# Optimization experiments

Measured on AMD Instinct MI355X. Metric: run time of the kernel, lower is better.

The kernel has to match this reference:

```python
import jax, jax.numpy as jnp
import numpy as np

B, S, D, H = 8, 1024, 1024, 16
HD = D // H  # head_dim = 64


def setup_inputs() -> dict:
    key = jax.random.key(0)
    ks = jax.random.split(key, 5)
    scale = 1.0 / np.sqrt(D)
    return {
        "x": jax.random.normal(ks[0], (B, S, D), dtype=jnp.float32),
        "wq": jax.random.normal(ks[1], (D, D), dtype=jnp.float32) * scale,
        "wk": jax.random.normal(ks[2], (D, D), dtype=jnp.float32) * scale,
        "wv": jax.random.normal(ks[3], (D, D), dtype=jnp.float32) * scale,
        "wo": jax.random.normal(ks[4], (D, D), dtype=jnp.float32) * scale,
    }


def reference(x, wq, wk, wv, wo):
    b, s, d = x.shape
    # nn.Linear: y = x @ W.T  (weights stored [out, in])
    q = (x @ wq.T).reshape(b, s, H, HD).transpose(0, 2, 1, 3)  # [b,h,s,hd]
    k = (x @ wk.T).reshape(b, s, H, HD).transpose(0, 2, 1, 3)
    v = (x @ wv.T).reshape(b, s, H, HD).transpose(0, 2, 1, 3)
    scores = jnp.einsum("bhqd,bhkd->bhqk", q, k) / jnp.sqrt(jnp.float32(HD))
    attn = jax.nn.softmax(scores, axis=-1)  # dropout p=0.0 -> identity
    out = jnp.einsum("bhqk,bhkd->bhqd", attn, v)
    out = out.transpose(0, 2, 1, 3).reshape(b, s, d)
    return out @ wo.T
```

## Files before the change

kernel.cpp:

```cpp
#include <hip/hip_runtime.h>
#include <hip/hip_bf16.h>
#include <math.h>

#define BB 8
#define SS 1024
#define DD 1024
#define HH 16
#define HDIM 64
#define MM (BB * SS)
#define QSCALE 0.1803368801111204f

typedef __attribute__((ext_vector_type(8))) short s8v;
typedef __attribute__((ext_vector_type(4))) short s4v;
typedef __attribute__((ext_vector_type(4))) float f4v;

#define GLD16(g, l)                                                            \
  __builtin_amdgcn_global_load_lds(                                            \
      (const __attribute__((address_space(1))) void*)(g),                      \
      (__attribute__((address_space(3))) void*)(l), 16, 0, 0)

__device__ __forceinline__ unsigned short bf16_ru(float f) {
  return (unsigned short)((__float_as_uint(f) + 0x8000u) >> 16);
}

__global__ void cast_kernel(const float* __restrict__ in,
                            __hip_bfloat16* __restrict__ out, int n) {
  int i = blockIdx.x * blockDim.x + threadIdx.x;
  int stride = gridDim.x * blockDim.x;
  for (int idx = i * 4; idx < n; idx += stride * 4) {
    float4 f = *(const float4*)&in[idx];
    out[idx + 0] = __float2bfloat16(f.x);
    out[idx + 1] = __float2bfloat16(f.y);
    out[idx + 2] = __float2bfloat16(f.z);
    out[idx + 3] = __float2bfloat16(f.w);
  }
}

template <int MODE>
__global__ __launch_bounds__(256, 2) void gemm_bt(
    const __hip_bfloat16* __restrict__ A, const __hip_bfloat16* __restrict__ Bm,
    float* __restrict__ Cf, __hip_bfloat16* __restrict__ Qo,
    __hip_bfloat16* __restrict__ Ko, __hip_bfloat16* __restrict__ Vt) {
  __shared__ __hip_bfloat16 sA[128 * 32];
  __shared__ __hip_bfloat16 sB[128 * 32];

  const int tid = threadIdx.x;
  const int wave = tid >> 6;
  const int lane = tid & 63;
  const int l15 = lane & 15;
  const int quad = lane >> 4;

  const int m0 = blockIdx.y * 128;
  const int n0 = blockIdx.x * 128;
  const int wm = (wave >> 1) * 64;
  const int wn = (wave & 1) * 64;

  f4v acc[4][4];
#pragma unroll
  for (int i = 0; i < 4; ++i)
#pragma unroll
    for (int j = 0; j < 4; ++j) acc[i][j] = {0.f, 0.f, 0.f, 0.f};

  for (int kt = 0; kt < DD / 32; ++kt) {
    const int k0 = kt * 32;
    __syncthreads();
#pragma unroll
    for (int r = 0; r < 2; ++r) {
      int e = r * 2048 + tid * 8;
      int row = e >> 5, col = e & 31;
      GLD16(A + (size_t)(m0 + row) * DD + k0 + col, &sA[r * 2048 + wave * 512]);
      GLD16(Bm + (size_t)(n0 + row) * DD + k0 + col, &sB[r * 2048 + wave * 512]);
    }
    __syncthreads();

    s8v af[4], bf[4];
#pragma unroll
    for (int i = 0; i < 4; ++i)
      af[i] = *(const s8v*)&sA[(wm + i * 16 + l15) * 32 + quad * 8];
#pragma unroll
    for (int j = 0; j < 4; ++j)
      bf[j] = *(const s8v*)&sB[(wn + j * 16 + l15) * 32 + quad * 8];
#pragma unroll
    for (int i = 0; i < 4; ++i)
#pragma unroll
      for (int j = 0; j < 4; ++j)
        acc[i][j] =
            __builtin_amdgcn_mfma_f32_16x16x32_bf16(af[i], bf[j], acc[i][j], 0, 0, 0);
  }

#pragma unroll
  for (int i = 0; i < 4; ++i) {
#pragma unroll
    for (int j = 0; j < 4; ++j) {
      const int rowb = m0 + wm + i * 16 + quad * 4;
      const int colb = n0 + wn + j * 16 + l15;
      if (MODE == 0) {
        int which = colb >> 10, hcol = colb & 1023;
        int h = hcol >> 6, hd = hcol & 63;
        int b = rowb >> 10, s = rowb & 1023;
        if (which == 2) {
          unsigned short us[4];
#pragma unroll
          for (int rg = 0; rg < 4; ++rg) us[rg] = bf16_ru(acc[i][j][rg]);
          uint2 pk = {(unsigned)us[0] | ((unsigned)us[1] << 16),
                      (unsigned)us[2] | ((unsigned)us[3] << 16)};
          *(uint2*)&Vt[((size_t)(b * HH + h) * HDIM + hd) * SS + s] = pk;
        } else if (which == 0) {
#pragma unroll
          for (int rg = 0; rg < 4; ++rg)
            ((unsigned short*)Qo)[((size_t)(b * HH + h) * SS + s + rg) * HDIM + hd] =
                bf16_ru(acc[i][j][rg] * QSCALE);
        } else {
#pragma unroll
          for (int rg = 0; rg < 4; ++rg)
            ((unsigned short*)Ko)[((size_t)(b * HH + h) * SS + s + rg) * HDIM + hd] =
                bf16_ru(acc[i][j][rg]);
        }
      } else {
#pragma unroll
        for (int rg = 0; rg < 4; ++rg)
          Cf[(size_t)(rowb + rg) * DD + colb] = acc[i][j][rg];
      }
    }
  }
}

#define SPLD 68
__global__ __launch_bounds__(256, 4) void attn_kernel(
    const __hip_bfloat16* __restrict__ Q, const __hip_bfloat16* __restrict__ K,
    const __hip_bfloat16* __restrict__ Vt, __hip_bfloat16* __restrict__ Oout) {
  __shared__ __hip_bfloat16 sK[64 * 64];
  __shared__ __hip_bfloat16 sVt[64 * 64];
  __shared__ unsigned short sP[4 * 32 * SPLD];

  const int tid = threadIdx.x;
  const int wave = tid >> 6;
  const int lane = tid & 63;
  const int l15 = lane & 15;
  const int quad = lane >> 4;
  const int c8 = lane & 7;
  const int r8 = lane >> 3;

  const int bh = blockIdx.x;
  const int q0 = blockIdx.y * 128;
  const size_t head = (size_t)bh * SS * HDIM;

  unsigned short* sPw = &sP[wave * 32 * SPLD];

  s8v qf[2][2];
#pragma unroll
  for (int mf = 0; mf < 2; ++mf) {
    int s = q0 + wave * 32 + mf * 16 + l15;
#pragma unroll
    for (int kk = 0; kk < 2; ++kk)
      qf[mf][kk] = *(const s8v*)&Q[head + (size_t)s * HDIM + kk * 32 + quad * 8];
  }

  s8v onesB;
#pragma unroll
  for (int j = 0; j < 8; ++j) onesB[j] = (short)0x3F80;

  f4v o[2][4];
  f4v lacc[2];
#pragma unroll
  for (int mf = 0; mf < 2; ++mf) {
    lacc[mf] = {0.f, 0.f, 0.f, 0.f};
#pragma unroll
    for (int f = 0; f < 4; ++f) o[mf][f] = {0.f, 0.f, 0.f, 0.f};
  }

  for (int kb = 0; kb < SS / 64; ++kb) {
    __syncthreads();
#pragma unroll
    for (int r = 0; r < 2; ++r) {
      int rb = r * 32 + wave * 8;
      int row = rb + r8;
      int sc8 = (c8 ^ (row & 7)) * 8;
      GLD16(&K[head + (size_t)(kb * 64 + row) * HDIM + sc8], &sK[rb * 64]);
      GLD16(&Vt[head + (size_t)row * SS + kb * 64 + sc8], &sVt[rb * 64]);
    }
    __syncthreads();

    f4v sc[2][4];
#pragma unroll
    for (int mf = 0; mf < 2; ++mf)
#pragma unroll
      for (int f = 0; f < 4; ++f) sc[mf][f] = {0.f, 0.f, 0.f, 0.f};
#pragma unroll
    for (int kk = 0; kk < 2; ++kk) {
#pragma unroll
      for (int f = 0; f < 4; ++f) {
        s8v kf = *(const s8v*)&sK[(f * 16 + l15) * 64 +
                                  (((kk * 4 + quad) ^ (l15 & 7)) * 8)];
#pragma unroll
        for (int mf = 0; mf < 2; ++mf)
          sc[mf][f] =
              __builtin_amdgcn_mfma_f32_16x16x32_bf16(qf[mf][kk], kf, sc[mf][f], 0, 0, 0);
      }
    }

#pragma unroll
    for (int mf = 0; mf < 2; ++mf)
#pragma unroll
      for (int f = 0; f < 4; ++f)
#pragma unroll
        for (int r = 0; r < 4; ++r)
          sPw[(mf * 16 + quad * 4 + r) * SPLD + f * 16 + l15] =
              bf16_ru(exp2f(sc[mf][f][r]));

#pragma unroll
    for (int kk = 0; kk < 2; ++kk) {
      s8v pf[2];
#pragma unroll
      for (int mf = 0; mf < 2; ++mf) {
        const unsigned short* p = &sPw[(mf * 16 + l15) * SPLD + kk * 32 + quad * 8];
        s4v lo = *(const s4v*)p;
        s4v hi = *(const s4v*)(p + 4);
        pf[mf] = __builtin_shufflevector(lo, hi, 0, 1, 2, 3, 4, 5, 6, 7);
        lacc[mf] = __builtin_amdgcn_mfma_f32_16x16x32_bf16(pf[mf], onesB, lacc[mf], 0, 0, 0);
      }
#pragma unroll
      for (int f = 0; f < 4; ++f) {
        s8v vf = *(const s8v*)&sVt[(f * 16 + l15) * 64 +
                                   (((kk * 4 + quad) ^ (l15 & 7)) * 8)];
#pragma unroll
        for (int mf = 0; mf < 2; ++mf)
          o[mf][f] =
              __builtin_amdgcn_mfma_f32_16x16x32_bf16(pf[mf], vf, o[mf][f], 0, 0, 0);
      }
    }
  }

  const int b = bh >> 4, h = bh & 15;
#pragma unroll
  for (int mf = 0; mf < 2; ++mf) {
    float rl[4];
#pragma unroll
    for (int r = 0; r < 4; ++r) rl[r] = 1.0f / lacc[mf][r];
#pragma unroll
    for (int f = 0; f < 4; ++f)
#pragma unroll
      for (int r = 0; r < 4; ++r) {
        int srow = q0 + wave * 32 + mf * 16 + quad * 4 + r;
        int col = h * HDIM + f * 16 + l15;
        ((unsigned short*)Oout)[(size_t)(b * SS + srow) * DD + col] =
            bf16_ru(o[mf][f][r] * rl[r]);
      }
  }
}

extern "C" void kernel_launch(void* const* d_in, const int* in_sizes, int n_in,
                              void* d_out, int out_size, void* d_ws, size_t ws_size,
                              hipStream_t stream) {
  const float* x = (const float*)d_in[0];
  const float* wq = (const float*)d_in[1];
  const float* wk = (const float*)d_in[2];
  const float* wv = (const float*)d_in[3];
  const float* wo = (const float*)d_in[4];

  char* ws = (char*)d_ws;
  __hip_bfloat16* xb = (__hip_bfloat16*)(ws);
  __hip_bfloat16* wqkvb = (__hip_bfloat16*)(ws + (16 << 20));
  __hip_bfloat16* wob = (__hip_bfloat16*)(ws + (22 << 20));
  __hip_bfloat16* qh = (__hip_bfloat16*)(ws + (24 << 20));
  __hip_bfloat16* kh = (__hip_bfloat16*)(ws + (40 << 20));
  __hip_bfloat16* vt = (__hip_bfloat16*)(ws + (56 << 20));
  __hip_bfloat16* attnO = (__hip_bfloat16*)(ws + (72 << 20));

  cast_kernel<<<2048, 256, 0, stream>>>(x, xb, MM * DD);
  cast_kernel<<<512, 256, 0, stream>>>(wq, wqkvb, DD * DD);
  cast_kernel<<<512, 256, 0, stream>>>(wk, wqkvb + DD * DD, DD * DD);
  cast_kernel<<<512, 256, 0, stream>>>(wv, wqkvb + 2 * DD * DD, DD * DD);
  cast_kernel<<<512, 256, 0, stream>>>(wo, wob, DD * DD);

  gemm_bt<0><<<dim3(24, 64), 256, 0, stream>>>(xb, wqkvb, nullptr, qh, kh, vt);

  attn_kernel<<<dim3(BB * HH, SS / 128), 256, 0, stream>>>(qh, kh, vt, attnO);

  gemm_bt<1><<<dim3(8, 64), 256, 0, stream>>>(attnO, wob, (float*)d_out, nullptr,
                                              nullptr, nullptr);
}
```

Before: 255.9 us.

## Fuse cast kernels and swap MFMA operands for vectorized epilogue stores

Replaces five cast launches with one fused kernel that writes packed bf16 pairs. It also swaps MFMA operand order in the GEMM, for the Q/K and output tiles, and in the attention QK^T step, so each lane holds four contiguous columns. That lets Q/K, the fp32 output and the P tile be written with 8- or 16-byte vector stores instead of scattered 2- or 4-byte stores. The P buffer row pitch changes to suit the new access pattern. This adds a branch on tile type in the GEMM and some code duplication.

```diff
diff --git a/kernel.cpp b/kernel.cpp
--- a/kernel.cpp
+++ b/kernel.cpp
@@ -23,16 +23,34 @@
   return (unsigned short)((__float_as_uint(f) + 0x8000u) >> 16);
 }
 
-__global__ void cast_kernel(const float* __restrict__ in,
-                            __hip_bfloat16* __restrict__ out, int n) {
-  int i = blockIdx.x * blockDim.x + threadIdx.x;
-  int stride = gridDim.x * blockDim.x;
-  for (int idx = i * 4; idx < n; idx += stride * 4) {
-    float4 f = *(const float4*)&in[idx];
-    out[idx + 0] = __float2bfloat16(f.x);
-    out[idx + 1] = __float2bfloat16(f.y);
-    out[idx + 2] = __float2bfloat16(f.z);
-    out[idx + 3] = __float2bfloat16(f.w);
+__global__ void cast_all(const float* __restrict__ x, const float* __restrict__ wq,
+                         const float* __restrict__ wk, const float* __restrict__ wv,
+                         const float* __restrict__ wo, __hip_bfloat16* __restrict__ xb,
+                         __hip_bfloat16* __restrict__ wqkvb,
+                         __hip_bfloat16* __restrict__ wob) {
+  int blk = blockIdx.x;
+  const float* src;
+  __hip_bfloat16* dst;
+  int base;
+  if (blk < 2048) {
+    src = x; dst = xb; base = blk * 4096;
+  } else if (blk < 2304) {
+    src = wq; dst = wqkvb; base = (blk - 2048) * 4096;
+  } else if (blk < 2560) {
+    src = wk; dst = wqkvb + (1 << 20); base = (blk - 2304) * 4096;
+  } else if (blk < 2816) {
+    src = wv; dst = wqkvb + (2 << 20); base = (blk - 2560) * 4096;
+  } else {
+    src = wo; dst = wob; base = (blk - 2816) * 4096;
+  }
+#pragma unroll
+  for (int it = 0; it < 4; ++it) {
+    int idx = base + it * 1024 + threadIdx.x * 4;
+    float4 f = *(const float4*)&src[idx];
+    unsigned short u0 = bf16_ru(f.x), u1 = bf16_ru(f.y);
+    unsigned short u2 = bf16_ru(f.z), u3 = bf16_ru(f.w);
+    *(uint2*)&dst[idx] = uint2{(unsigned)u0 | ((unsigned)u1 << 16),
+                               (unsigned)u2 | ((unsigned)u3 << 16)};
   }
 }
 
@@ -55,6 +73,8 @@
   const int wm = (wave >> 1) * 64;
   const int wn = (wave & 1) * 64;
 
+  const bool swapT = (MODE == 1) || (n0 < 2048);
+
   f4v acc[4][4];
 #pragma unroll
   for (int i = 0; i < 4; ++i)
@@ -80,58 +100,70 @@
 #pragma unroll
     for (int j = 0; j < 4; ++j)
       bf[j] = *(const s8v*)&sB[(wn + j * 16 + l15) * 32 + quad * 8];
-#pragma unroll
-    for (int i = 0; i < 4; ++i)
-#pragma unroll
-      for (int j = 0; j < 4; ++j)
-        acc[i][j] =
-            __builtin_amdgcn_mfma_f32_16x16x32_bf16(af[i], bf[j], acc[i][j], 0, 0, 0);
+    if (swapT) {
+#pragma unroll
+      for (int i = 0; i < 4; ++i)
+#pragma unroll
+        for (int j = 0; j < 4; ++j)
+          acc[i][j] =
+              __builtin_amdgcn_mfma_f32_16x16x32_bf16(bf[j], af[i], acc[i][j], 0, 0, 0);
+    } else {
+#pragma unroll
+      for (int i = 0; i < 4; ++i)
+#pragma unroll
+        for (int j = 0; j < 4; ++j)
+          acc[i][j] =
+              __builtin_amdgcn_mfma_f32_16x16x32_bf16(af[i], bf[j], acc[i][j], 0, 0, 0);
+    }
   }
 
 #pragma unroll
   for (int i = 0; i < 4; ++i) {
 #pragma unroll
     for (int j = 0; j < 4; ++j) {
-      const int rowb = m0 + wm + i * 16 + quad * 4;
-      const int colb = n0 + wn + j * 16 + l15;
-      if (MODE == 0) {
-        int which = colb >> 10, hcol = colb & 1023;
+      if (swapT) {
+        const int s_abs = m0 + wm + i * 16 + l15;
+        const int col = n0 + wn + j * 16 + quad * 4;
+        if (MODE == 0) {
+          int which = col >> 10, hcol = col & 1023;
+          int h = hcol >> 6, hd = hcol & 63;
+          int b = s_abs >> 10, s = s_abs & 1023;
+          float scl = (which == 0) ? QSCALE : 1.0f;
+          unsigned short us[4];
+#pragma unroll
+          for (int rg = 0; rg < 4; ++rg) us[rg] = bf16_ru(acc[i][j][rg] * scl);
+          __hip_bfloat16* dst = (which == 0) ? Qo : Ko;
+          *(uint2*)&dst[((size_t)(b * HH + h) * SS + s) * HDIM + hd] =
+              uint2{(unsigned)us[0] | ((unsigned)us[1] << 16),
+                    (unsigned)us[2] | ((unsigned)us[3] << 16)};
+        } else {
+          float4 f4 = {acc[i][j][0], acc[i][j][1], acc[i][j][2], acc[i][j][3]};
+          *(float4*)&Cf[(size_t)s_abs * DD + col] = f4;
+        }
+      } else {
+        const int rowb = m0 + wm + i * 16 + quad * 4;
+        const int colb = n0 + wn + j * 16 + l15;
+        int hcol = colb & 1023;
         int h = hcol >> 6, hd = hcol & 63;
         int b = rowb >> 10, s = rowb & 1023;
-        if (which == 2) {
-          unsigned short us[4];
-#pragma unroll
-          for (int rg = 0; rg < 4; ++rg) us[rg] = bf16_ru(acc[i][j][rg]);
-          uint2 pk = {(unsigned)us[0] | ((unsigned)us[1] << 16),
-                      (unsigned)us[2] | ((unsigned)us[3] << 16)};
-          *(uint2*)&Vt[((size_t)(b * HH + h) * HDIM + hd) * SS + s] = pk;
-        } else if (which == 0) {
-#pragma unroll
-          for (int rg = 0; rg < 4; ++rg)
-            ((unsigned short*)Qo)[((size_t)(b * HH + h) * SS + s + rg) * HDIM + hd] =
-                bf16_ru(acc[i][j][rg] * QSCALE);
-        } else {
-#pragma unroll
-          for (int rg = 0; rg < 4; ++rg)
-            ((unsigned short*)Ko)[((size_t)(b * HH + h) * SS + s + rg) * HDIM + hd] =
-                bf16_ru(acc[i][j][rg]);
-        }
-      } else {
-#pragma unroll
-        for (int rg = 0; rg < 4; ++rg)
-          Cf[(size_t)(rowb + rg) * DD + colb] = acc[i][j][rg];
-      }
-    }
-  }
-}
-
-#define SPLD 68
+        unsigned short us[4];
+#pragma unroll
+        for (int rg = 0; rg < 4; ++rg) us[rg] = bf16_ru(acc[i][j][rg]);
+        *(uint2*)&Vt[((size_t)(b * HH + h) * HDIM + hd) * SS + s] =
+            uint2{(unsigned)us[0] | ((unsigned)us[1] << 16),
+                  (unsigned)us[2] | ((unsigned)us[3] << 16)};
+      }
+    }
+  }
+}
+
+#define KPLD 76
 __global__ __launch_bounds__(256, 4) void attn_kernel(
     const __hip_bfloat16* __restrict__ Q, const __hip_bfloat16* __restrict__ K,
     const __hip_bfloat16* __restrict__ Vt, __hip_bfloat16* __restrict__ Oout) {
   __shared__ __hip_bfloat16 sK[64 * 64];
   __shared__ __hip_bfloat16 sVt[64 * 64];
-  __shared__ unsigned short sP[4 * 32 * SPLD];
+  __shared__ unsigned short sP[4 * 32 * KPLD];
 
   const int tid = threadIdx.x;
   const int wave = tid >> 6;
@@ -145,7 +177,7 @@
   const int q0 = blockIdx.y * 128;
   const size_t head = (size_t)bh * SS * HDIM;
 
-  unsigned short* sPw = &sP[wave * 32 * SPLD];
+  unsigned short* sPw = &sP[wave * 32 * KPLD];
 
   s8v qf[2][2];
 #pragma unroll
@@ -195,25 +227,28 @@
 #pragma unroll
         for (int mf = 0; mf < 2; ++mf)
           sc[mf][f] =
-              __builtin_amdgcn_mfma_f32_16x16x32_bf16(qf[mf][kk], kf, sc[mf][f], 0, 0, 0);
+              __builtin_amdgcn_mfma_f32_16x16x32_bf16(kf, qf[mf][kk], sc[mf][f], 0, 0, 0);
       }
     }
 
 #pragma unroll
     for (int mf = 0; mf < 2; ++mf)
 #pragma unroll
-      for (int f = 0; f < 4; ++f)
-#pragma unroll
-        for (int r = 0; r < 4; ++r)
-          sPw[(mf * 16 + quad * 4 + r) * SPLD + f * 16 + l15] =
-              bf16_ru(exp2f(sc[mf][f][r]));
+      for (int f = 0; f < 4; ++f) {
+        unsigned short us[4];
+#pragma unroll
+        for (int r = 0; r < 4; ++r) us[r] = bf16_ru(exp2f(sc[mf][f][r]));
+        *(uint2*)&sPw[(mf * 16 + l15) * KPLD + f * 16 + quad * 4] =
+            uint2{(unsigned)us[0] | ((unsigned)us[1] << 16),
+                  (unsigned)us[2] | ((unsigned)us[3] << 16)};
+      }
 
 #pragma unroll
     for (int kk = 0; kk < 2; ++kk) {
       s8v pf[2];
 #pragma unroll
       for (int mf = 0; mf < 2; ++mf) {
-        const unsigned short* p = &sPw[(mf * 16 + l15) * SPLD + kk * 32 + quad * 8];
+        const unsigned short* p = &sPw[(mf * 16 + l15) * KPLD + kk * 32 + quad * 8];
         s4v lo = *(const s4v*)p;
         s4v hi = *(const s4v*)(p + 4);
         pf[mf] = __builtin_shufflevector(lo, hi, 0, 1, 2, 3, 4, 5, 6, 7);
@@ -267,11 +302,7 @@
   __hip_bfloat16* vt = (__hip_bfloat16*)(ws + (56 << 20));
   __hip_bfloat16* attnO = (__hip_bfloat16*)(ws + (72 << 20));
 
-  cast_kernel<<<2048, 256, 0, stream>>>(x, xb, MM * DD);
-  cast_kernel<<<512, 256, 0, stream>>>(wq, wqkvb, DD * DD);
-  cast_kernel<<<512, 256, 0, stream>>>(wk, wqkvb + DD * DD, DD * DD);
-  cast_kernel<<<512, 256, 0, stream>>>(wv, wqkvb + 2 * DD * DD, DD * DD);
-  cast_kernel<<<512, 256, 0, stream>>>(wo, wob, DD * DD);
+  cast_all<<<3072, 256, 0, stream>>>(x, wq, wk, wv, wo, xb, wqkvb, wob);
 
   gemm_bt<0><<<dim3(24, 64), 256, 0, stream>>>(xb, wqkvb, nullptr, qh, kh, vt);
 
```

After: 256.0 us. Within noise of the previous version (+0.0%).
